# Optimization experiments

Hardware: AMD Instinct MI355X
Metric: run time of the kernel (lower is better)

Reference implementation:

```python
import jax, jax.numpy as jnp
import numpy as np

EXP_BITS = 5
SIG_BITS = 10


def fp_quantize_ste(x, exp_bits=EXP_BITS, sig_bits=SIG_BITS):
    """Simulate a low-precision float format (round-to-nearest, subnormals on),
    with a straight-through estimator for gradients."""
    ebias = 2 ** (exp_bits - 1) - 1
    emin = 1 - ebias                      # min normal exponent; below -> subnormal
    emax = ebias
    xmax = (2.0 - 2.0 ** (-sig_bits)) * (2.0 ** emax)

    ax = jnp.abs(x)
    # exponent of each value; guard log2(0)
    e = jnp.floor(jnp.log2(jnp.where(ax > 0, ax, 1.0)))
    # clamping e below emin quantizes subnormals on the fixed 2^(emin-sig_bits) grid;
    # clamping above emax is handled by the final saturation to +-xmax
    e = jnp.clip(e, emin, emax)
    scale = jnp.exp2(sig_bits - e)        # quantization step = 2^(e - sig_bits)
    q = jnp.round(x * scale) / scale      # round-to-nearest (rmode=1)
    q = jnp.clip(q, -xmax, xmax)
    q = jnp.where(ax > 0, q, x)           # preserve exact zeros (and signed zero)
    # straight-through estimator: forward = q, backward = identity
    return x + jax.lax.stop_gradient(q - x)


def setup_inputs() -> dict:
    key = jax.random.key(0)
    k1, k2, k3 = jax.random.split(key, 3)
    N, D_IN, D_OUT = 8192, 4096, 4096
    x = jax.random.normal(k1, (N, D_IN), dtype=jnp.float32)
    weight = jax.random.normal(k2, (D_OUT, D_IN), dtype=jnp.float32) * (D_IN ** -0.5)
    bias = jax.random.normal(k3, (D_OUT,), dtype=jnp.float32) * 0.01
    return {"x": x, "weight": weight, "bias": bias}


def reference(x, weight, bias):
    xq = fp_quantize_ste(x)               # act_quant
    wq = fp_quantize_ste(weight)          # weight_quant
    bq = fp_quantize_ste(bias)            # bias quantized with weight_quant
    # F.linear: x @ W^T + b
    return jnp.einsum('ni,oi->no', xq, wq) + bq
```

## Files before the change

kernel.cpp:

```cpp
#include <hip/hip_runtime.h>
#include <hip/hip_fp16.h>
#include <cstdint>
#include <cstddef>

#define GLOBAL_AS __attribute__((address_space(1)))
#define LDS_AS    __attribute__((address_space(3)))

typedef __attribute__((ext_vector_type(8))) _Float16 f16x8;
typedef __attribute__((ext_vector_type(4))) float    f32x4;

__device__ __forceinline__ void gload_lds16(const void* g, void* l) {
    __builtin_amdgcn_global_load_lds((const GLOBAL_AS void*)g,
                                     (LDS_AS void*)l, 16, 0, 0);
}

__device__ __forceinline__ __half qcvt(float x) {
    x = fminf(fmaxf(x, -65504.f), 65504.f);
    return __float2half(x);
}

__global__ void quant_xw_f32_to_f16(const float* __restrict__ xin, int x4,
                                    const float* __restrict__ win, int w4,
                                    __half* __restrict__ xout,
                                    __half* __restrict__ wout) {
    const int stride = gridDim.x * blockDim.x;
    const int tot = x4 + w4;
    for (int i = blockIdx.x * blockDim.x + threadIdx.x; i < tot; i += stride) {
        const bool isx = (i < x4);
        const int  j   = isx ? i : i - x4;
        const float4 f = reinterpret_cast<const float4*>(isx ? xin : win)[j];
        union { __half h[4]; uint2 u; } p;
        p.h[0] = qcvt(f.x);
        p.h[1] = qcvt(f.y);
        p.h[2] = qcvt(f.z);
        p.h[3] = qcvt(f.w);
        reinterpret_cast<uint2*>(isx ? xout : wout)[j] = p.u;
    }
}

__global__ __launch_bounds__(512, 2) void gemm_f16_8phase(
    const __half* __restrict__ A, const __half* __restrict__ B,
    const float* __restrict__ bias, float* __restrict__ C,
    int M, int N, int K)
{
    __shared__ __align__(16) __half lds[2][2][2][8192];

    const int tid  = threadIdx.x;
    const int lane = tid & 63;
    const int wid  = tid >> 6;
    const int wr   = wid >> 2;
    const int wc   = wid & 3;
    const int fr   = lane & 15;
    const int fq   = lane >> 4;

    const int nwg = gridDim.x;
    const int qq = nwg >> 3, rr = nwg & 7;
    const int xcd = blockIdx.x & 7, idx = blockIdx.x >> 3;
    const int wgid = (xcd < rr ? xcd * (qq + 1)
                               : rr * (qq + 1) + (xcd - rr) * qq) + idx;
    const int nbn = N >> 8;
    const int tile_m = (wgid / nbn) << 8;
    const int tile_n = (wgid % nbn) << 8;

    const int wbyte = (lane * 16) ^ (((lane >> 5) & 1) << 5);
    const int srow  = ((wid >> 1) << 4) + (wbyte >> 6);
    const int scb   = ((wid & 1) << 6) + (wbyte & 63);
    const char* gA0 = (const char*)A + (size_t)(tile_m + srow) * K * 2 + scb;
    const char* gB0 = (const char*)B + (size_t)(tile_n + srow) * K * 2 + scb;
    const size_t rstep = (size_t)64  * K * 2;
    const size_t hstep = (size_t)128 * K * 2;
    const int ldst = tid * 16;

    const int woff = (fr * 64 + fq * 16) ^ (((fr >> 3) & 1) << 5);
    const uint32_t lds0 = (uint32_t)(size_t)(LDS_AS const char*)&lds[0][0][0][0];
    const uint32_t aBase = lds0 + (uint32_t)(wr * 8192 + woff);
    const uint32_t bBase = lds0 + 32768u + (uint32_t)(wc * 4096 + woff);

    f32x4 acc[2][2][4][2];
#pragma unroll
    for (int qa = 0; qa < 2; ++qa)
#pragma unroll
        for (int qb = 0; qb < 2; ++qb)
#pragma unroll
            for (int m = 0; m < 4; ++m)
#pragma unroll
                for (int n = 0; n < 2; ++n)
                    acc[qa][qb][m][n] = (f32x4){0.f, 0.f, 0.f, 0.f};

    f16x8 af[4][2];
    f16x8 bfP[2][2];
    f16x8 bfQ[2][2];

#define STAGE_A(bufi, h, kt) do {                                          \
        char* l_ = (char*)(&lds[bufi][0][h][0]) + ldst;                    \
        const char* g_ = gA0 + (size_t)(kt) * 128 + ((h) ? hstep : 0);     \
        gload_lds16(g_, l_);                                               \
        gload_lds16(g_ + rstep, l_ + 8192);                                \
    } while (0)

#define STAGE_B(bufi, h, kt) do {                                          \
        char* l_ = (char*)(&lds[bufi][1][h][0]) + ldst;                    \
        const char* g_ = gB0 + (size_t)(kt) * 128 + ((h) ? hstep : 0);     \
        gload_lds16(g_, l_);                                               \
        gload_lds16(g_ + rstep, l_ + 8192);                                \
    } while (0)

#define DSR(dst, addr, OFF)                                                \
    asm volatile("ds_read_b128 %0, %1 offset:" OFF                         \
                 : "=v"(dst) : "v"(addr))

#define LDGA(bufi, qa) do {                                                \
        const uint32_t a_ = aBase + (bufi) * 65536u + (qa) * 16384u;       \
        DSR(af[0][0], a_, "0");    DSR(af[0][1], a_, "1024");              \
        DSR(af[1][0], a_, "2048"); DSR(af[1][1], a_, "3072");              \
        DSR(af[2][0], a_, "4096"); DSR(af[2][1], a_, "5120");              \
        DSR(af[3][0], a_, "6144"); DSR(af[3][1], a_, "7168");              \
    } while (0)

#define LDGB(dst, bufi, hb) do {                                           \
        const uint32_t b_ = bBase + (bufi) * 65536u + (hb) * 16384u;       \
        DSR(dst[0][0], b_, "0");    DSR(dst[0][1], b_, "1024");            \
        DSR(dst[1][0], b_, "2048"); DSR(dst[1][1], b_, "3072");            \
    } while (0)

#define MMA_PAIR(qa, qb, mm, nn, BF)                                       \
    acc[qa][qb][mm][nn] = __builtin_amdgcn_mfma_f32_16x16x32_f16(          \
        af[mm][0], BF[nn][0], acc[qa][qb][mm][nn], 0, 0, 0);               \
    acc[qa][qb][mm][nn] = __builtin_amdgcn_mfma_f32_16x16x32_f16(          \
        af[mm][1], BF[nn][1], acc[qa][qb][mm][nn], 0, 0, 0);

#define MMA_M01(qa, qb, BF)                                                \
    __builtin_amdgcn_s_setprio(1);                                         \
    MMA_PAIR(qa, qb, 0, 0, BF) MMA_PAIR(qa, qb, 0, 1, BF)                  \
    MMA_PAIR(qa, qb, 1, 0, BF) MMA_PAIR(qa, qb, 1, 1, BF)                  \
    __builtin_amdgcn_s_setprio(0);

#define MMA_M23(qa, qb, BF)                                                \
    __builtin_amdgcn_s_setprio(1);                                         \
    MMA_PAIR(qa, qb, 2, 0, BF) MMA_PAIR(qa, qb, 2, 1, BF)                  \
    MMA_PAIR(qa, qb, 3, 0, BF) MMA_PAIR(qa, qb, 3, 1, BF)                  \
    __builtin_amdgcn_s_setprio(0);

#define MMA_N0(qa, qb, BF)                                                 \
    __builtin_amdgcn_s_setprio(1);                                         \
    MMA_PAIR(qa, qb, 0, 0, BF) MMA_PAIR(qa, qb, 1, 0, BF)                  \
    MMA_PAIR(qa, qb, 2, 0, BF) MMA_PAIR(qa, qb, 3, 0, BF)                  \
    __builtin_amdgcn_s_setprio(0);

#define MMA_N1(qa, qb, BF)                                                 \
    __builtin_amdgcn_s_setprio(1);                                         \
    MMA_PAIR(qa, qb, 0, 1, BF) MMA_PAIR(qa, qb, 1, 1, BF)                  \
    MMA_PAIR(qa, qb, 2, 1, BF) MMA_PAIR(qa, qb, 3, 1, BF)                  \
    __builtin_amdgcn_s_setprio(0);

#define MMA_FULL(qa, qb, BF)                                               \
    MMA_M01(qa, qb, BF) MMA_M23(qa, qb, BF)

#define WAITL(NLIT)                                                        \
    asm volatile("s_waitcnt lgkmcnt(" NLIT ")");                           \
    __builtin_amdgcn_sched_barrier(0)

#define BARS()                                                             \
    __builtin_amdgcn_s_barrier();                                          \
    __builtin_amdgcn_sched_barrier(0)

#define TILE_FULL(cur, nxt, kt, B0S, B1S)                                  \
                \
    LDGA(cur, 0); STAGE_B(nxt, 0, (kt) + 1);                               \
    WAITL("4"); MMA_M01(0, 0, B0S);                                        \
    WAITL("0"); MMA_M23(0, 0, B0S);                                        \
    BARS();                                                                \
                    \
    LDGB(B1S, cur, 1); STAGE_A(cur, 0, (kt) + 2);                          \
    WAITL("2"); MMA_N0(0, 1, B1S);                                         \
    WAITL("0"); MMA_N1(0, 1, B1S);                                         \
    BARS();                                                                \
                \
    LDGA(cur, 1); STAGE_B(cur, 1, (kt) + 2);                               \
    WAITL("4"); MMA_M01(1, 1, B1S);                                        \
    WAITL("0"); MMA_M23(1, 1, B1S);                                        \
    BARS();                                                                \
    \
    STAGE_A(cur, 1, (kt) + 2);                                             \
    asm volatile("s_waitcnt vmcnt(6)");                                    \
    BARS();                                                                \
    LDGB(B1S, nxt, 0);                                                     \
    __builtin_amdgcn_sched_barrier(0);                                     \
    MMA_FULL(1, 0, B0S);                                                   \
    BARS();

    STAGE_A(0, 0, 0); STAGE_B(0, 0, 0); STAGE_B(0, 1, 0); STAGE_A(0, 1, 0);
    STAGE_A(1, 0, 1); STAGE_B(1, 1, 1); STAGE_A(1, 1, 1);
    asm volatile("s_waitcnt vmcnt(6)");
    BARS();
    LDGB(bfP, 0, 0);

    const int nt = K >> 6;
    for (int kt = 0; kt + 3 < nt; kt += 2) {
        TILE_FULL(0, 1, kt,     bfP, bfQ);
        TILE_FULL(1, 0, kt + 1, bfQ, bfP);
    }

    LDGA(0, 0); STAGE_B(1, 0, nt - 1);
    WAITL("4"); MMA_M01(0, 0, bfP);
    WAITL("0"); MMA_M23(0, 0, bfP);
    BARS();
    LDGB(bfQ, 0, 1);
    WAITL("2"); MMA_N0(0, 1, bfQ);
    WAITL("0"); MMA_N1(0, 1, bfQ);
    BARS();
    LDGA(0, 1);
    WAITL("4"); MMA_M01(1, 1, bfQ);
    WAITL("0"); MMA_M23(1, 1, bfQ);
    BARS();
    asm volatile("s_waitcnt vmcnt(0)");
    BARS();
    LDGB(bfQ, 1, 0);
    __builtin_amdgcn_sched_barrier(0);
    MMA_FULL(1, 0, bfP);
    BARS();

    LDGA(1, 0);
    WAITL("4"); MMA_M01(0, 0, bfQ);
    WAITL("0"); MMA_M23(0, 0, bfQ);
    BARS();
    LDGB(bfP, 1, 1);
    WAITL("2"); MMA_N0(0, 1, bfP);
    WAITL("0"); MMA_N1(0, 1, bfP);
    BARS();
    LDGA(1, 1);
    WAITL("4"); MMA_M01(1, 1, bfP);
    WAITL("0"); MMA_M23(1, 1, bfP);
    BARS();
    MMA_FULL(1, 0, bfQ);

    float bv[2][2];
#pragma unroll
    for (int qb = 0; qb < 2; ++qb)
#pragma unroll
        for (int n = 0; n < 2; ++n)
            bv[qb][n] = __half2float(qcvt(
                bias[tile_n + qb * 128 + wc * 32 + n * 16 + fr]));

#pragma unroll
    for (int qa = 0; qa < 2; ++qa)
#pragma unroll
        for (int qb = 0; qb < 2; ++qb)
#pragma unroll
            for (int m = 0; m < 4; ++m)
#pragma unroll
                for (int n = 0; n < 2; ++n) {
                    const int col = tile_n + qb * 128 + wc * 32 + n * 16 + fr;
                    const int rowb = tile_m + qa * 128 + wr * 64 + m * 16 + fq * 4;
#pragma unroll
                    for (int r = 0; r < 4; ++r)
                        C[(size_t)(rowb + r) * N + col] =
                            acc[qa][qb][m][n][r] + bv[qb][n];
                }

#undef STAGE_A
#undef STAGE_B
#undef DSR
#undef LDGA
#undef LDGB
#undef MMA_PAIR
#undef MMA_M01
#undef MMA_M23
#undef MMA_N0
#undef MMA_N1
#undef MMA_FULL
#undef WAITL
#undef BARS
#undef TILE_FULL
}

__global__ void qat_gemm_naive(const float* __restrict__ A,
                               const float* __restrict__ B,
                               const float* __restrict__ bias,
                               float* __restrict__ C, int M, int N, int K) {
    const int col = blockIdx.x * blockDim.x + threadIdx.x;
    const int row = blockIdx.y;
    if (col >= N || row >= M) return;
    float s = 0.f;
    for (int k = 0; k < K; ++k) {
        float a = __half2float(qcvt(A[(size_t)row * K + k]));
        float b = __half2float(qcvt(B[(size_t)col * K + k]));
        s += a * b;
    }
    C[(size_t)row * N + col] = s + __half2float(qcvt(bias[col]));
}

extern "C" void kernel_launch(void* const* d_in, const int* in_sizes, int n_in,
                              void* d_out, int out_size, void* d_ws,
                              size_t ws_size, hipStream_t stream) {
    const float* x = (const float*)d_in[0];
    const float* w = (const float*)d_in[1];
    const float* b = (const float*)d_in[2];
    float* out = (float*)d_out;

    const int xn = in_sizes[0];
    const int wn = in_sizes[1];
    const int N  = in_sizes[2];
    const int K  = wn / N;
    const int M  = xn / K;

    const size_t need = (size_t)(xn + wn) * sizeof(__half);
    const bool ok = (M % 256 == 0) && (N % 256 == 0) &&
                    (K % 128 == 0) && (K >= 256);

    if (ws_size >= need && ok) {
        __half* xq = (__half*)d_ws;
        __half* wq = xq + xn;

        const int x4 = xn / 4, w4 = wn / 4;
        int blk = ((x4 + w4) + 255) / 256; if (blk > 2048) blk = 2048;
        quant_xw_f32_to_f16<<<blk, 256, 0, stream>>>(x, x4, w, w4, xq, wq);

        dim3 grid((M / 256) * (N / 256));
        gemm_f16_8phase<<<grid, 512, 0, stream>>>(xq, wq, b, out, M, N, K);
    } else {
        dim3 grid((N + 255) / 256, M);
        qat_gemm_naive<<<grid, 256, 0, stream>>>(x, w, b, out, M, N, K);
    }
}
```

Baseline: 276.1 us.

## Double-buffer A fragments in registers and prefetch LDS reads earlier

Adds a second register set for the A-operand fragments so LDS reads for the next quadrant and the next k-tile are issued one phase ahead of the MFMAs that consume them. The MFMA groups are rebalanced into finer per-m chunks with graded lgkmcnt waits, aiming to hide LDS read latency behind matrix math. The cost is more VGPRs, which may lower occupancy or cause spills. An unused PHASE0 macro is also left in.

```diff
diff --git a/kernel.cpp b/kernel.cpp
--- a/kernel.cpp
+++ b/kernel.cpp
@@ -87,9 +87,10 @@
                 for (int n = 0; n < 2; ++n)
                     acc[qa][qb][m][n] = (f32x4){0.f, 0.f, 0.f, 0.f};
 
-    f16x8 af[4][2];
-    f16x8 bfP[2][2];
-    f16x8 bfQ[2][2];
+    f16x8 afX[4][2];
+    f16x8 afY[4][2];
+    f16x8 bfU[2][2];
+    f16x8 bfV[2][2];
 
 #define STAGE_A(bufi, h, kt) do {                                          \
         char* l_ = (char*)(&lds[bufi][0][h][0]) + ldst;                    \
@@ -109,12 +110,12 @@
     asm volatile("ds_read_b128 %0, %1 offset:" OFF                         \
                  : "=v"(dst) : "v"(addr))
 
-#define LDGA(bufi, qa) do {                                                \
+#define LDGA(dst, bufi, qa) do {                                           \
         const uint32_t a_ = aBase + (bufi) * 65536u + (qa) * 16384u;       \
-        DSR(af[0][0], a_, "0");    DSR(af[0][1], a_, "1024");              \
-        DSR(af[1][0], a_, "2048"); DSR(af[1][1], a_, "3072");              \
-        DSR(af[2][0], a_, "4096"); DSR(af[2][1], a_, "5120");              \
-        DSR(af[3][0], a_, "6144"); DSR(af[3][1], a_, "7168");              \
+        DSR(dst[0][0], a_, "0");    DSR(dst[0][1], a_, "1024");            \
+        DSR(dst[1][0], a_, "2048"); DSR(dst[1][1], a_, "3072");            \
+        DSR(dst[2][0], a_, "4096"); DSR(dst[2][1], a_, "5120");            \
+        DSR(dst[3][0], a_, "6144"); DSR(dst[3][1], a_, "7168");            \
     } while (0)
 
 #define LDGB(dst, bufi, hb) do {                                           \
@@ -123,38 +124,24 @@
         DSR(dst[1][0], b_, "2048"); DSR(dst[1][1], b_, "3072");            \
     } while (0)
 
-#define MMA_PAIR(qa, qb, mm, nn, BF)                                       \
+#define MMA_PAIR(qa, qb, mm, nn, AF, BF)                                   \
     acc[qa][qb][mm][nn] = __builtin_amdgcn_mfma_f32_16x16x32_f16(          \
-        af[mm][0], BF[nn][0], acc[qa][qb][mm][nn], 0, 0, 0);               \
+        AF[mm][0], BF[nn][0], acc[qa][qb][mm][nn], 0, 0, 0);               \
     acc[qa][qb][mm][nn] = __builtin_amdgcn_mfma_f32_16x16x32_f16(          \
-        af[mm][1], BF[nn][1], acc[qa][qb][mm][nn], 0, 0, 0);
-
-#define MMA_M01(qa, qb, BF)                                                \
+        AF[mm][1], BF[nn][1], acc[qa][qb][mm][nn], 0, 0, 0);
+
+#define MMA_Q(qa, qb, mm, AF, BF)                                          \
     __builtin_amdgcn_s_setprio(1);                                         \
-    MMA_PAIR(qa, qb, 0, 0, BF) MMA_PAIR(qa, qb, 0, 1, BF)                  \
-    MMA_PAIR(qa, qb, 1, 0, BF) MMA_PAIR(qa, qb, 1, 1, BF)                  \
+    MMA_PAIR(qa, qb, mm, 0, AF, BF) MMA_PAIR(qa, qb, mm, 1, AF, BF)        \
     __builtin_amdgcn_s_setprio(0);
 
-#define MMA_M23(qa, qb, BF)                                                \
+#define MMA_FULL(qa, qb, AF, BF)                                           \
     __builtin_amdgcn_s_setprio(1);                                         \
-    MMA_PAIR(qa, qb, 2, 0, BF) MMA_PAIR(qa, qb, 2, 1, BF)                  \
-    MMA_PAIR(qa, qb, 3, 0, BF) MMA_PAIR(qa, qb, 3, 1, BF)                  \
+    MMA_PAIR(qa, qb, 0, 0, AF, BF) MMA_PAIR(qa, qb, 0, 1, AF, BF)          \
+    MMA_PAIR(qa, qb, 1, 0, AF, BF) MMA_PAIR(qa, qb, 1, 1, AF, BF)          \
+    MMA_PAIR(qa, qb, 2, 0, AF, BF) MMA_PAIR(qa, qb, 2, 1, AF, BF)          \
+    MMA_PAIR(qa, qb, 3, 0, AF, BF) MMA_PAIR(qa, qb, 3, 1, AF, BF)          \
     __builtin_amdgcn_s_setprio(0);
-
-#define MMA_N0(qa, qb, BF)                                                 \
-    __builtin_amdgcn_s_setprio(1);                                         \
-    MMA_PAIR(qa, qb, 0, 0, BF) MMA_PAIR(qa, qb, 1, 0, BF)                  \
-    MMA_PAIR(qa, qb, 2, 0, BF) MMA_PAIR(qa, qb, 3, 0, BF)                  \
-    __builtin_amdgcn_s_setprio(0);
-
-#define MMA_N1(qa, qb, BF)                                                 \
-    __builtin_amdgcn_s_setprio(1);                                         \
-    MMA_PAIR(qa, qb, 0, 1, BF) MMA_PAIR(qa, qb, 1, 1, BF)                  \
-    MMA_PAIR(qa, qb, 2, 1, BF) MMA_PAIR(qa, qb, 3, 1, BF)                  \
-    __builtin_amdgcn_s_setprio(0);
-
-#define MMA_FULL(qa, qb, BF)                                               \
-    MMA_M01(qa, qb, BF) MMA_M23(qa, qb, BF)
 
 #define WAITL(NLIT)                                                        \
     asm volatile("s_waitcnt lgkmcnt(" NLIT ")");                           \
@@ -164,75 +151,85 @@
     __builtin_amdgcn_s_barrier();                                          \
     __builtin_amdgcn_sched_barrier(0)
 
-#define TILE_FULL(cur, nxt, kt, B0S, B1S)                                  \
-                \
-    LDGA(cur, 0); STAGE_B(nxt, 0, (kt) + 1);                               \
-    WAITL("4"); MMA_M01(0, 0, B0S);                                        \
-    WAITL("0"); MMA_M23(0, 0, B0S);                                        \
+#define PHASE0(SU, SV, STMT)                                               \
+    STMT;                                                                  \
+    LDGB(SV, 99, 99);                          \
+    BARS()
+
+#define TILE_FULL(cur, nxt, kt, SU, SV)                                    \
+              \
+    STAGE_B(nxt, 0, (kt) + 1);                                             \
+    LDGB(SV, cur, 1);                                                      \
+    WAITL("10"); MMA_Q(0, 0, 0, afX, SU);                                  \
+    WAITL("8");  MMA_Q(0, 0, 1, afX, SU);                                  \
+    WAITL("6");  MMA_Q(0, 0, 2, afX, SU);                                  \
+    WAITL("4");  MMA_Q(0, 0, 3, afX, SU);                                  \
     BARS();                                                                \
-                    \
-    LDGB(B1S, cur, 1); STAGE_A(cur, 0, (kt) + 2);                          \
-    WAITL("2"); MMA_N0(0, 1, B1S);                                         \
-    WAITL("0"); MMA_N1(0, 1, B1S);                                         \
+             \
+    STAGE_A(cur, 0, (kt) + 2);                                             \
+    LDGA(afY, cur, 1);                                                     \
+    WAITL("8"); MMA_FULL(0, 1, afX, SV);                                   \
     BARS();                                                                \
-                \
-    LDGA(cur, 1); STAGE_B(cur, 1, (kt) + 2);                               \
-    WAITL("4"); MMA_M01(1, 1, B1S);                                        \
-    WAITL("0"); MMA_M23(1, 1, B1S);                                        \
+                                  \
+    STAGE_B(cur, 1, (kt) + 2);                                             \
+    WAITL("0"); MMA_FULL(1, 1, afY, SV);                                   \
     BARS();                                                                \
-    \
+      \
     STAGE_A(cur, 1, (kt) + 2);                                             \
     asm volatile("s_waitcnt vmcnt(6)");                                    \
     BARS();                                                                \
-    LDGB(B1S, nxt, 0);                                                     \
+    LDGB(SV, nxt, 0);                                                      \
+    LDGA(afX, nxt, 0);                                                     \
     __builtin_amdgcn_sched_barrier(0);                                     \
-    MMA_FULL(1, 0, B0S);                                                   \
+    MMA_FULL(1, 0, afY, SU);                                               \
     BARS();
 
     STAGE_A(0, 0, 0); STAGE_B(0, 0, 0); STAGE_B(0, 1, 0); STAGE_A(0, 1, 0);
     STAGE_A(1, 0, 1); STAGE_B(1, 1, 1); STAGE_A(1, 1, 1);
     asm volatile("s_waitcnt vmcnt(6)");
     BARS();
-    LDGB(bfP, 0, 0);
+    LDGB(bfU, 0, 0);
+    LDGA(afX, 0, 0);
+    __builtin_amdgcn_sched_barrier(0);
 
     const int nt = K >> 6;
     for (int kt = 0; kt + 3 < nt; kt += 2) {
-        TILE_FULL(0, 1, kt,     bfP, bfQ);
-        TILE_FULL(1, 0, kt + 1, bfQ, bfP);
+        TILE_FULL(0, 1, kt,     bfU, bfV);
+        TILE_FULL(1, 0, kt + 1, bfV, bfU);
     }
 
-    LDGA(0, 0); STAGE_B(1, 0, nt - 1);
-    WAITL("4"); MMA_M01(0, 0, bfP);
-    WAITL("0"); MMA_M23(0, 0, bfP);
-    BARS();
-    LDGB(bfQ, 0, 1);
-    WAITL("2"); MMA_N0(0, 1, bfQ);
-    WAITL("0"); MMA_N1(0, 1, bfQ);
-    BARS();
-    LDGA(0, 1);
-    WAITL("4"); MMA_M01(1, 1, bfQ);
-    WAITL("0"); MMA_M23(1, 1, bfQ);
+    STAGE_B(1, 0, nt - 1);
+    LDGB(bfV, 0, 1);
+    WAITL("10"); MMA_Q(0, 0, 0, afX, bfU);
+    WAITL("8");  MMA_Q(0, 0, 1, afX, bfU);
+    WAITL("6");  MMA_Q(0, 0, 2, afX, bfU);
+    WAITL("4");  MMA_Q(0, 0, 3, afX, bfU);
+    BARS();
+    LDGA(afY, 0, 1);
+    WAITL("8"); MMA_FULL(0, 1, afX, bfV);
+    BARS();
+    WAITL("0"); MMA_FULL(1, 1, afY, bfV);
     BARS();
     asm volatile("s_waitcnt vmcnt(0)");
     BARS();
-    LDGB(bfQ, 1, 0);
+    LDGB(bfV, 1, 0);
+    LDGA(afX, 1, 0);
     __builtin_amdgcn_sched_barrier(0);
-    MMA_FULL(1, 0, bfP);
-    BARS();
-
-    LDGA(1, 0);
-    WAITL("4"); MMA_M01(0, 0, bfQ);
-    WAITL("0"); MMA_M23(0, 0, bfQ);
-    BARS();
-    LDGB(bfP, 1, 1);
-    WAITL("2"); MMA_N0(0, 1, bfP);
-    WAITL("0"); MMA_N1(0, 1, bfP);
-    BARS();
-    LDGA(1, 1);
-    WAITL("4"); MMA_M01(1, 1, bfP);
-    WAITL("0"); MMA_M23(1, 1, bfP);
-    BARS();
-    MMA_FULL(1, 0, bfQ);
+    MMA_FULL(1, 0, afY, bfU);
+    BARS();
+
+    LDGB(bfU, 1, 1);
+    WAITL("10"); MMA_Q(0, 0, 0, afX, bfV);
+    WAITL("8");  MMA_Q(0, 0, 1, afX, bfV);
+    WAITL("6");  MMA_Q(0, 0, 2, afX, bfV);
+    WAITL("4");  MMA_Q(0, 0, 3, afX, bfV);
+    BARS();
+    LDGA(afY, 1, 1);
+    WAITL("8"); MMA_FULL(0, 1, afX, bfU);
+    BARS();
+    WAITL("0"); MMA_FULL(1, 1, afY, bfU);
+    BARS();
+    MMA_FULL(1, 0, afY, bfV);
 
     float bv[2][2];
 #pragma unroll
@@ -264,14 +261,12 @@
 #undef LDGA
 #undef LDGB
 #undef MMA_PAIR
-#undef MMA_M01
-#undef MMA_M23
-#undef MMA_N0
-#undef MMA_N1
+#undef MMA_Q
 #undef MMA_FULL
 #undef WAITL
 #undef BARS
 #undef TILE_FULL
+#undef PHASE0
 }
 
 __global__ void qat_gemm_naive(const float* __restrict__ A,
```

Measured after the change: 405.8 us. 1.47x slower.
